# Optimization experiments

Measured on AMD Instinct MI355X. Metric: run time of the kernel, lower is better.

The kernel has to match this reference:

```python
import jax, jax.numpy as jnp
import numpy as np
import math

CHANNELS = 128
NUM_NODES = 170
LENGTH = 12
BATCH = 128


def setup_inputs() -> dict:
    key = jax.random.key(0)
    k_x, k_es = jax.random.split(key)
    x = jax.random.normal(k_x, (BATCH, CHANNELS, NUM_NODES, LENGTH), dtype=jnp.float32)
    # xavier_uniform for E_s [channels, num_nodes]
    bound = math.sqrt(6.0 / (CHANNELS + NUM_NODES))
    E_s = jax.random.uniform(k_es, (CHANNELS, NUM_NODES), dtype=jnp.float32,
                             minval=-bound, maxval=bound)
    return {"x": x, "E_s": E_s}


def reference(x, E_s):
    # x: [B, C, N, T], E_s: [C, M] with M == N (num_nodes)
    # Note: the original also computes E_t = x * E_tod**2, which is dead code
    # (never used in the returned value), so it is omitted here.
    C = x.shape[1]
    # node embeddings: sum over channel and time -> [B, N, M]
    E_d = jnp.tanh(jnp.einsum('bcnt,cm->bnm', x, E_s))
    # node-node similarity: contract over the M (embedding) axis -> [B, N, N]
    scores = jax.nn.relu(jnp.einsum('bnm,bkm->bnk', E_d, E_d) / jnp.sqrt(jnp.float32(C)))
    A_adp = jax.nn.softmax(scores, axis=-1)  # [B, N, N]
    A_mean = A_adp.mean(axis=0)              # [N, N]
    return (A_mean > 0.5).astype(jnp.float32)
```

## Files before the change

### kernel.cpp

```cpp
#include <hip/hip_runtime.h>
#include <math.h>

#define NB 128
#define NC 128
#define NN 170
#define NT 12
#define NP 192
#define MP 176

#define EST_SZ ((size_t)NP * NC)
#define P_SZ   ((size_t)NB * NN * MP)

typedef _Float16 h8 __attribute__((ext_vector_type(8)));
typedef float    f4 __attribute__((ext_vector_type(4)));

__device__ __forceinline__ float fast_tanh(float x) {
    float cx = fminf(fmaxf(x, -15.f), 15.f);
    float e  = __expf(2.f * cx);
    return (e - 1.f) * __builtin_amdgcn_rcpf(e + 1.f);
}

__global__ __launch_bounds__(256) void kprep_est(const float* __restrict__ Es,
                                                 _Float16* __restrict__ Est) {
    int idx = blockIdx.x * 256 + threadIdx.x;
    int m = idx >> 7, c = idx & 127;
    Est[idx] = (m < NN) ? (_Float16)Es[c * NN + m] : (_Float16)0.f;
}

#define ATSW(row, c)  ((row) * 128 + (((((c) >> 3) ^ ((row) & 7)) << 3) | ((c) & 7)))
#define EDSW(row, m)  ((row) * 192 + (((((m) >> 3) ^ ((row) & 7)) << 3) | ((m) & 7)))
#define SCSTR 204

__global__ __launch_bounds__(1024) void kA_fused(const float* __restrict__ x,
                                                 const _Float16* __restrict__ Est,
                                                 _Float16* __restrict__ P) {
    const int h = blockIdx.x, b = blockIdx.y;
    const int r0 = h * 96;
    const int t = threadIdx.x;
    const int lane = t & 63, wave = t >> 6;
    const int l15 = lane & 15, quad = lane >> 4;
    const int wr = wave >> 2, wc = wave & 3;

    __shared__ __align__(16) float    L[16 * 510];
    __shared__ __align__(16) char     UN[192 * 128 * 2];
    __shared__ __align__(16) _Float16 EdL[192 * 192];
    _Float16* At = (_Float16*)UN;
    float*    Sc = (float*)UN;

    const float4* xb = reinterpret_cast<const float4*>(x + (size_t)b * NC * NN * NT);
    for (int r8 = 0; r8 < 8; ++r8) {
        float4 vv[8];
        #pragma unroll
        for (int it = 0; it < 8; ++it) {
            int s = t + it * 1024;
            vv[it] = (s < 8160) ? xb[(size_t)r8 * 8160 + s]
                                : make_float4(0.f, 0.f, 0.f, 0.f);
        }
        #pragma unroll
        for (int it = 0; it < 8; ++it) {
            int s = t + it * 1024;
            if (s < 8160)
                L[s] = (vv[it].x + vv[it].y) + (vv[it].z + vv[it].w);
        }
        __syncthreads();
        #pragma unroll
        for (int it = 0; it < 3; ++it) {
            int idx = t + it * 1024;
            int n = idx >> 4, cc = idx & 15;
            float s = 0.f;
            if (n < NN)
                s = L[cc * 510 + 3 * n] + L[cc * 510 + 3 * n + 1]
                  + L[cc * 510 + 3 * n + 2];
            At[ATSW(n, r8 * 16 + cc)] = (_Float16)s;
        }
        __syncthreads();
    }

    {
        f4 acc1[3][3] = {};
        #pragma unroll
        for (int kk = 0; kk < 4; ++kk) {
            int ks = kk * 32 + quad * 8;
            h8 a[3], bf[3];
            #pragma unroll
            for (int rt = 0; rt < 3; ++rt) {
                int row = wr * 48 + rt * 16 + l15;
                a[rt] = *reinterpret_cast<const h8*>(
                    &At[row * 128 + (((ks >> 3) ^ (row & 7)) << 3)]);
            }
            #pragma unroll
            for (int ci = 0; ci < 3; ++ci) {
                int m = wc * 48 + ci * 16 + l15;
                bf[ci] = *reinterpret_cast<const h8*>(Est + (size_t)m * NC + ks);
            }
            #pragma unroll
            for (int rt = 0; rt < 3; ++rt)
                #pragma unroll
                for (int ci = 0; ci < 3; ++ci)
                    acc1[rt][ci] = __builtin_amdgcn_mfma_f32_16x16x32_f16(
                        a[rt], bf[ci], acc1[rt][ci], 0, 0, 0);
        }
        #pragma unroll
        for (int rt = 0; rt < 3; ++rt)
            #pragma unroll
            for (int ci = 0; ci < 3; ++ci) {
                int m = wc * 48 + ci * 16 + l15;
                #pragma unroll
                for (int reg = 0; reg < 4; ++reg) {
                    int n = wr * 48 + rt * 16 + quad * 4 + reg;
                    EdL[EDSW(n, m)] = (_Float16)fast_tanh(acc1[rt][ci][reg]);
                }
            }
    }
    __syncthreads();

    f4 acc2[3][3] = {};
    if (wave < 8) {
        const int gr = wave >> 2, gc = wave & 3;
        #pragma unroll 2
        for (int mc = 0; mc < 192; mc += 32) {
            int mg = (mc >> 3) + quad;
            h8 a2[3], b2[3];
            #pragma unroll
            for (int rt = 0; rt < 3; ++rt) {
                int row = r0 + gr * 48 + rt * 16 + l15;
                a2[rt] = *reinterpret_cast<const h8*>(
                    &EdL[row * 192 + ((mg ^ (row & 7)) << 3)]);
            }
            #pragma unroll
            for (int ci = 0; ci < 3; ++ci) {
                int row = gc * 48 + ci * 16 + l15;
                b2[ci] = *reinterpret_cast<const h8*>(
                    &EdL[row * 192 + ((mg ^ (row & 7)) << 3)]);
            }
            #pragma unroll
            for (int rt = 0; rt < 3; ++rt)
                #pragma unroll
                for (int ci = 0; ci < 3; ++ci)
                    acc2[rt][ci] = __builtin_amdgcn_mfma_f32_16x16x32_f16(
                        a2[rt], b2[ci], acc2[rt][ci], 0, 0, 0);
        }
    }

    const float scale = 0.08838834764831845f;
    for (int p = 0; p < 2; ++p) {
        __syncthreads();
        if (wave < 8 && (wave >> 2) == p) {
            const int gc = wave & 3;
            #pragma unroll
            for (int rt = 0; rt < 3; ++rt)
                #pragma unroll
                for (int ci = 0; ci < 3; ++ci) {
                    int col = gc * 48 + ci * 16 + l15;
                    #pragma unroll
                    for (int reg = 0; reg < 4; ++reg) {
                        int rloc = rt * 16 + quad * 4 + reg;
                        Sc[rloc * SCSTR + col] = fmaxf(acc2[rt][ci][reg] * scale, 0.f);
                    }
                }
        }
        __syncthreads();
        #pragma unroll
        for (int rr = 0; rr < 3; ++rr) {
            int r = wave * 3 + rr;
            int n = r0 + p * 48 + r;
            if (n >= NN) continue;
            float v0 = Sc[r * SCSTR + lane];
            float v1 = Sc[r * SCSTR + lane + 64];
            int  k2i = lane + 128;
            bool has2 = (k2i < NN);
            float v2 = has2 ? Sc[r * SCSTR + k2i] : -1.f;
            float m = fmaxf(fmaxf(v0, v1), v2);
            #pragma unroll
            for (int off = 32; off; off >>= 1) m = fmaxf(m, __shfl_xor(m, off, 64));
            float e0 = __expf(v0 - m);
            float e1 = __expf(v1 - m);
            float e2 = has2 ? __expf(v2 - m) : 0.f;
            float s = e0 + e1 + e2;
            #pragma unroll
            for (int off = 32; off; off >>= 1) s += __shfl_xor(s, off, 64);
            float inv = 1.f / s;
            _Float16* Pr = P + ((size_t)(b * NN + n)) * MP;
            Pr[lane]      = (_Float16)(e0 * inv);
            Pr[lane + 64] = (_Float16)(e1 * inv);
            if (has2) Pr[k2i] = (_Float16)(e2 * inv);
        }
    }
}

__global__ __launch_bounds__(256) void k4_mean_thresh(const _Float16* __restrict__ P,
                                                      float* __restrict__ out) {
    int p = blockIdx.x * 256 + threadIdx.x;
    if (p >= NN * NN) return;
    int n = p / NN, k = p - n * NN;
    const _Float16* base = P + (size_t)n * MP + k;
    float s0 = 0.f, s1 = 0.f, s2 = 0.f, s3 = 0.f;
    #pragma unroll
    for (int b = 0; b < NB; b += 4) {
        s0 += (float)base[(size_t)(b + 0) * NN * MP];
        s1 += (float)base[(size_t)(b + 1) * NN * MP];
        s2 += (float)base[(size_t)(b + 2) * NN * MP];
        s3 += (float)base[(size_t)(b + 3) * NN * MP];
    }
    float s = (s0 + s1) + (s2 + s3);
    out[p] = (s * (1.f / 128.f) > 0.5f) ? 1.f : 0.f;
}

extern "C" void kernel_launch(void* const* d_in, const int* in_sizes, int n_in,
                              void* d_out, int out_size, void* d_ws, size_t ws_size,
                              hipStream_t stream) {
    const float* x  = (const float*)d_in[0];
    const float* Es = (const float*)d_in[1];
    float* out = (float*)d_out;

    _Float16* Est = (_Float16*)d_ws;
    _Float16* P   = Est + EST_SZ;

    kprep_est<<<96, 256, 0, stream>>>(Es, Est);
    kA_fused<<<dim3(2, 128), 1024, 0, stream>>>(x, Est, P);
    k4_mean_thresh<<<113, 256, 0, stream>>>(P, out);
}
```

Before: 219.5 us.

## Double-buffer x channel reduction with register prefetch and single barrier per step

The x-load stage of the fused kernel now processes 8 channels per step over 16 steps. It uses two LDS buffers and prefetches the next step's global loads into registers before the barrier, so one barrier per step replaces two. This is meant to overlap HBM latency with the LDS reduction and cut synchronisation. The mean/threshold kernel also gets 8 independent accumulators instead of 4 to expose more memory-level parallelism. The raw s_barrier with a manual lgkmcnt wait relies on the double buffer to avoid write-after-read hazards.

```diff
diff --git a/kernel.cpp b/kernel.cpp
--- a/kernel.cpp
+++ b/kernel.cpp
@@ -41,40 +41,52 @@
     const int l15 = lane & 15, quad = lane >> 4;
     const int wr = wave >> 2, wc = wave & 3;
 
-    __shared__ __align__(16) float    L[16 * 510];
+    __shared__ __align__(16) float    Lb[2 * 4080];
     __shared__ __align__(16) char     UN[192 * 128 * 2];
     __shared__ __align__(16) _Float16 EdL[192 * 192];
     _Float16* At = (_Float16*)UN;
     float*    Sc = (float*)UN;
 
     const float4* xb = reinterpret_cast<const float4*>(x + (size_t)b * NC * NN * NT);
-    for (int r8 = 0; r8 < 8; ++r8) {
-        float4 vv[8];
-        #pragma unroll
-        for (int it = 0; it < 8; ++it) {
+    float4 vv[4];
+    #pragma unroll
+    for (int it = 0; it < 4; ++it) {
+        int s = t + it * 1024;
+        vv[it] = (s < 4080) ? xb[s] : make_float4(0.f, 0.f, 0.f, 0.f);
+    }
+    for (int r = 0; r < 16; ++r) {
+        const int cur = (r & 1) * 4080;
+        #pragma unroll
+        for (int it = 0; it < 4; ++it) {
             int s = t + it * 1024;
-            vv[it] = (s < 8160) ? xb[(size_t)r8 * 8160 + s]
-                                : make_float4(0.f, 0.f, 0.f, 0.f);
-        }
-        #pragma unroll
-        for (int it = 0; it < 8; ++it) {
-            int s = t + it * 1024;
-            if (s < 8160)
-                L[s] = (vv[it].x + vv[it].y) + (vv[it].z + vv[it].w);
-        }
-        __syncthreads();
-        #pragma unroll
-        for (int it = 0; it < 3; ++it) {
+            if (s < 4080)
+                Lb[cur + s] = (vv[it].x + vv[it].y) + (vv[it].z + vv[it].w);
+        }
+        if (r < 15) {
+            const float4* xr = xb + (size_t)(r + 1) * 4080;
+            #pragma unroll
+            for (int it = 0; it < 4; ++it) {
+                int s = t + it * 1024;
+                vv[it] = (s < 4080) ? xr[s] : make_float4(0.f, 0.f, 0.f, 0.f);
+            }
+        }
+        asm volatile("s_waitcnt lgkmcnt(0)" ::: "memory");
+        __builtin_amdgcn_s_barrier();
+        __builtin_amdgcn_sched_barrier(0);
+        #pragma unroll
+        for (int it = 0; it < 2; ++it) {
             int idx = t + it * 1024;
-            int n = idx >> 4, cc = idx & 15;
-            float s = 0.f;
-            if (n < NN)
-                s = L[cc * 510 + 3 * n] + L[cc * 510 + 3 * n + 1]
-                  + L[cc * 510 + 3 * n + 2];
-            At[ATSW(n, r8 * 16 + cc)] = (_Float16)s;
-        }
-        __syncthreads();
-    }
+            if (idx < 1536) {
+                int n = idx >> 3, cc = idx & 7;
+                float sv = 0.f;
+                if (n < NN)
+                    sv = Lb[cur + cc * 510 + 3 * n] + Lb[cur + cc * 510 + 3 * n + 1]
+                       + Lb[cur + cc * 510 + 3 * n + 2];
+                At[ATSW(n, r * 8 + cc)] = (_Float16)sv;
+            }
+        }
+    }
+    __syncthreads();
 
     {
         f4 acc1[3][3] = {};
@@ -195,14 +207,19 @@
     int n = p / NN, k = p - n * NN;
     const _Float16* base = P + (size_t)n * MP + k;
     float s0 = 0.f, s1 = 0.f, s2 = 0.f, s3 = 0.f;
+    float s4 = 0.f, s5 = 0.f, s6 = 0.f, s7 = 0.f;
     #pragma unroll
-    for (int b = 0; b < NB; b += 4) {
+    for (int b = 0; b < NB; b += 8) {
         s0 += (float)base[(size_t)(b + 0) * NN * MP];
         s1 += (float)base[(size_t)(b + 1) * NN * MP];
         s2 += (float)base[(size_t)(b + 2) * NN * MP];
         s3 += (float)base[(size_t)(b + 3) * NN * MP];
-    }
-    float s = (s0 + s1) + (s2 + s3);
+        s4 += (float)base[(size_t)(b + 4) * NN * MP];
+        s5 += (float)base[(size_t)(b + 5) * NN * MP];
+        s6 += (float)base[(size_t)(b + 6) * NN * MP];
+        s7 += (float)base[(size_t)(b + 7) * NN * MP];
+    }
+    float s = ((s0 + s1) + (s2 + s3)) + ((s4 + s5) + (s6 + s7));
     out[p] = (s * (1.f / 128.f) > 0.5f) ? 1.f : 0.f;
 }
 
```

Result: slower. 227.4 us (+3.6%).
